# Kernel optimization log

Measured on AMD Instinct MI355X. Metric: run time of the kernel, lower is better.

## Reference

```python
import jax, jax.numpy as jnp
import numpy as np

HIDDEN = 1024
HEADS = 16
HEAD = HIDDEN // HEADS


def setup_inputs() -> dict:
    key = jax.random.key(0)
    ks = jax.random.split(key, 6)
    B, T = 2, 2048
    x = jax.random.normal(ks[0], (B, T, HIDDEN), dtype=jnp.float32)
    mask = jnp.ones((T, T), dtype=jnp.float32)
    s = 1.0 / np.sqrt(HIDDEN)
    Wqkv = jax.random.normal(ks[1], (HIDDEN, 3 * HIDDEN), dtype=jnp.float32) * s
    bqkv = jnp.zeros((3 * HIDDEN,), dtype=jnp.float32)
    Wproj = jax.random.normal(ks[2], (HIDDEN, HIDDEN), dtype=jnp.float32) * s
    bproj = jnp.zeros((HIDDEN,), dtype=jnp.float32)
    return {"x": x, "mask": mask, "Wqkv": Wqkv, "bqkv": bqkv,
            "Wproj": Wproj, "bproj": bproj}


def reference(x, mask, Wqkv, bqkv, Wproj, bproj):
    B, T, C = x.shape
    qkv = x @ Wqkv + bqkv                      # [B,T,3C]
    q, k, v = jnp.split(qkv, 3, axis=-1)
    def heads(t):                              # [B,T,C] -> [B,H,T,D]
        return t.reshape(B, T, HEADS, HEAD).transpose(0, 2, 1, 3)
    q, k, v = heads(q), heads(k), heads(v)
    scores = jnp.einsum('bhqd,bhkd->bhqk', q, k) / np.sqrt(HEAD)
    scores = jnp.where(mask == 0, -jnp.inf, scores)
    attn = jax.nn.softmax(scores, axis=-1)
    out = jnp.einsum('bhqk,bhkd->bhqd', attn, v)
    out = out.transpose(0, 2, 1, 3).reshape(B, T, C)
    return out @ Wproj + bproj
```

## Files before the change

### kernel.cpp

```cpp
#include <hip/hip_runtime.h>
#include <stdint.h>

#define HID 1024
#define NH 16
#define HD 64
#define BATCH 2
#define SEQ 2048
#define MR (BATCH*SEQ)
#define NQKV (3*HID)

typedef __attribute__((ext_vector_type(8))) _Float16 h16x8;
typedef __attribute__((ext_vector_type(4))) _Float16 h16x4;
typedef __attribute__((ext_vector_type(2))) __fp16 fp16x2;
typedef __attribute__((ext_vector_type(8))) unsigned short u16x8;
typedef __attribute__((ext_vector_type(4))) float f32x4;

#if __has_builtin(__builtin_amdgcn_exp2f)
#define EXP2(x) __builtin_amdgcn_exp2f(x)
#else
#define EXP2(x) exp2f(x)
#endif

static __device__ __forceinline__ unsigned short f2h(float f) {
  union { _Float16 h; unsigned short u; } v; v.h = (_Float16)f; return v.u;
}
static __device__ __forceinline__ unsigned pk2(float a, float b) {
  union { fp16x2 h; unsigned u; } v;
  v.h = __builtin_amdgcn_cvt_pkrtz(a, b);
  return v.u;
}

typedef const __attribute__((address_space(1))) unsigned int glb_u32;
typedef __attribute__((address_space(3))) unsigned int lds_u32;
static __device__ __forceinline__ void cp16(const void* g, void* l) {
  __builtin_amdgcn_global_load_lds((glb_u32*)g, (lds_u32*)l, 16, 0, 0);
}

#define QSCL (0.125f * 1.44269504f)

__global__ __launch_bounds__(256) void k_prep(const float4* __restrict__ x4,
                                              const float* __restrict__ mask,
                                              const float* __restrict__ Wqkv,
                                              const float* __restrict__ Wproj,
                                              ushort4* __restrict__ xh,
                                              unsigned short* __restrict__ WqT,
                                              unsigned short* __restrict__ WpT,
                                              unsigned long long* __restrict__ mb) {
  __shared__ float tile[32][33];
  int blk = blockIdx.x, tid = threadIdx.x;
  if (blk < 4096) {
    int i = blk * 256 + tid;
    float4 v = x4[i];
    ushort4 h;
    h.x = f2h(v.x); h.y = f2h(v.y); h.z = f2h(v.z); h.w = f2h(v.w);
    xh[i] = h;
  } else if (blk < 8192) {
    const float* src; unsigned short* dst; int C, bx, by;
    if (blk < 7168) { src = Wqkv;  dst = WqT; C = NQKV; int b2 = blk - 4096; bx = b2 % 96; by = b2 / 96; }
    else            { src = Wproj; dst = WpT; C = HID;  int b2 = blk - 7168; bx = b2 & 31; by = b2 >> 5; }
    int tx = tid & 31, ty = tid >> 5;
    int col0 = bx * 32, row0 = by * 32;
    #pragma unroll
    for (int i = 0; i < 32; i += 8)
      tile[ty + i][tx] = src[(size_t)(row0 + ty + i) * C + col0 + tx];
    __syncthreads();
    #pragma unroll
    for (int i = 0; i < 32; i += 8)
      dst[(size_t)(col0 + ty + i) * HID + row0 + tx] = f2h(tile[tx][ty + i]);
  } else {
    int gw0 = (blk - 8192) * 16 + (tid >> 6) * 4;
    int lane = tid & 63;
    size_t base = (size_t)gw0 * 64;
    #pragma unroll
    for (int j = 0; j < 4; j++) {
      float v = mask[base + j * 64 + lane];
      unsigned long long b = __ballot(v != 0.f);
      if (lane == 0) mb[gw0 + j] = b;
    }
  }
}

__global__ __launch_bounds__(256) void k_gemm_qkv(const unsigned short* __restrict__ A,
                                                  const unsigned short* __restrict__ Bt,
                                                  const float* __restrict__ bias,
                                                  unsigned short* __restrict__ Qp,
                                                  unsigned short* __restrict__ Kp,
                                                  unsigned short* __restrict__ Vt) {
  const int K = HID;
  int tid = threadIdx.x;
  int wave = tid >> 6, lane = tid & 63, quad = lane >> 4, l16 = lane & 15;
  int wm = wave >> 1, wn = wave & 1;
  int x7 = l16 & 7;
  int lin = blockIdx.x + 24 * blockIdx.y;
  int orig = (lin & 7) * 96 + (lin >> 3);
  int m0 = (orig / 24) * 128, n0 = (orig % 24) * 128;
  __shared__ __align__(16) unsigned short smem[17408];
  unsigned short* As = smem;
  unsigned short* Bs = smem + 8192;
  unsigned short* Lb = smem;
  f32x4 acc[4][4] = {};
  for (int k0 = 0; k0 < K; k0 += 64) {
    __syncthreads();
    #pragma unroll
    for (int i = 0; i < 4; i++) {
      int c = tid + i * 256;
      int r = c >> 3, sc = ((c ^ r) & 7) << 3;
      cp16(&A[(size_t)(m0 + r) * K + k0 + sc], &As[c << 3]);
      cp16(&Bt[(size_t)(n0 + r) * K + k0 + sc], &Bs[c << 3]);
    }
    __syncthreads();
    #pragma unroll
    for (int kc = 0; kc < 2; kc++) {
      h16x8 af[4], bf[4];
      #pragma unroll
      for (int i = 0; i < 4; i++) {
        af[i] = *(const h16x8*)&As[(wm * 64 + i * 16 + l16) * 64 + (((kc * 4 + quad) ^ x7) << 3)];
        bf[i] = *(const h16x8*)&Bs[(wn * 64 + i * 16 + l16) * 64 + (((kc * 4 + quad) ^ x7) << 3)];
      }
      #pragma unroll
      for (int i = 0; i < 4; i++)
        #pragma unroll
        for (int j = 0; j < 4; j++)
          acc[i][j] = __builtin_amdgcn_mfma_f32_16x16x32_f16(af[i], bf[j], acc[i][j], 0, 0, 0);
    }
  }
  int which = n0 >> 10;
  int hbase = (n0 & 1023) >> 6;
  __syncthreads();
  if (which == 2) {
    #pragma unroll
    for (int j = 0; j < 4; j++) {
      int nl = wn * 64 + j * 16 + l16;
      float bv = bias[n0 + nl];
      #pragma unroll
      for (int i = 0; i < 4; i++) {
        int ml = wm * 64 + i * 16 + quad * 4;
        uint2 tt;
        tt.x = pk2(acc[i][j][0] + bv, acc[i][j][1] + bv);
        tt.y = pk2(acc[i][j][2] + bv, acc[i][j][3] + bv);
        *(uint2*)&Lb[nl * 136 + ml] = tt;
      }
    }
  } else {
    float scl = (which == 0) ? QSCL : 1.0f;
    #pragma unroll
    for (int j = 0; j < 4; j++) {
      int nl = wn * 64 + j * 16 + l16;
      float bv = bias[n0 + nl];
      #pragma unroll
      for (int i = 0; i < 4; i++)
        #pragma unroll
        for (int r = 0; r < 4; r++) {
          int ml = wm * 64 + i * 16 + quad * 4 + r;
          Lb[ml * 136 + nl] = f2h((acc[i][j][r] + bv) * scl);
        }
    }
  }
  __syncthreads();
  int b = m0 >> 11, tb = m0 & 2047;
  if (which == 2) {
    #pragma unroll
    for (int p = 0; p < 8; p++) {
      int c = tid + p * 256;
      int rr = c >> 4, cc = c & 15;
      int h = hbase + (rr >> 6), d = rr & 63;
      u16x8 vv = *(const u16x8*)&Lb[rr * 136 + cc * 8];
      *(u16x8*)&Vt[(size_t)(b * NH + h) * (SEQ * HD) + (size_t)d * SEQ + tb + cc * 8] = vv;
    }
  } else {
    unsigned short* dst = (which == 0) ? Qp : Kp;
    #pragma unroll
    for (int p = 0; p < 8; p++) {
      int c = tid + p * 256;
      int rr = c >> 4, cc = c & 15;
      int h = hbase + (cc >> 3), d0 = (cc & 7) << 3;
      u16x8 vv = *(const u16x8*)&Lb[rr * 136 + cc * 8];
      *(u16x8*)&dst[(size_t)(b * NH + h) * (SEQ * HD) + (size_t)(tb + rr) * HD + d0] = vv;
    }
  }
}

__global__ __launch_bounds__(256) void k_attn(const unsigned short* __restrict__ Qp,
                                              const unsigned short* __restrict__ Kp,
                                              const unsigned short* __restrict__ Vt,
                                              const unsigned long long* __restrict__ mb,
                                              unsigned short* __restrict__ AO) {
  int tid = threadIdx.x, wave = tid >> 6, lane = tid & 63, quad = lane >> 4, l16 = lane & 15;
  int lin = blockIdx.x + 16 * blockIdx.y;
  int orig = (lin & 7) * 64 + (lin >> 3);
  int bh = orig >> 4, qbase = (orig & 15) * 128;
  const unsigned short* Qg = Qp + (size_t)bh * (SEQ * HD);
  const unsigned short* Kg = Kp + (size_t)bh * (SEQ * HD);
  const unsigned short* Vg = Vt + (size_t)bh * (SEQ * HD);
  __shared__ __align__(16) unsigned short smem[24576];
  unsigned short* Qs = smem;
  unsigned short* Os = smem;

  #pragma unroll
  for (int i = 0; i < 4; i++) {
    int c = tid + i * 256;
    int row = c >> 3, sc = ((c ^ row) & 7) << 3;
    cp16(&Qg[(size_t)(qbase + row) * HD + sc], &Qs[c << 3]);
  }
  #pragma unroll
  for (int i = 0; i < 2; i++) {
    int c = tid + i * 256;
    int row = c >> 3, sc = ((c ^ row) & 7) << 3;
    cp16(&Kg[(size_t)row * HD + sc], &smem[8192 + (c << 3)]);
    cp16(&Vg[(size_t)row * SEQ + sc], &smem[12288 + (c << 3)]);
  }
  int q0 = qbase + wave * 32 + l16;
  const unsigned long long* mrow0 = mb + (size_t)q0 * 32;
  const unsigned long long* mrow1 = mb + (size_t)(q0 + 16) * 32;
  f32x4 acc_o[2][4] = {};
  f32x4 acc_l[2] = {};
  int x7 = l16 & 7;

  h16x4 vone4;
  #pragma unroll
  for (int j = 0; j < 4; j++) vone4[j] = (_Float16)1.0f;

  __syncthreads();
  h16x8 bq[2][2];
  #pragma unroll
  for (int s = 0; s < 2; s++)
    #pragma unroll
    for (int kk = 0; kk < 2; kk++)
      bq[s][kk] = *(const h16x8*)&Qs[(wave * 32 + s * 16 + l16) * 64 + (((kk * 4 + quad) ^ x7) << 3)];

  for (int kt = 0; kt < 32; kt++) {
    unsigned short* cb = smem + 8192 + ((kt & 1) << 13);
    if (kt < 31) {
      unsigned short* nb = smem + 8192 + (((kt + 1) & 1) << 13);
      int kb2 = (kt + 1) * 64;
      #pragma unroll
      for (int i = 0; i < 2; i++) {
        int c = tid + i * 256;
        int row = c >> 3, sc = ((c ^ row) & 7) << 3;
        cp16(&Kg[(size_t)(kb2 + row) * HD + sc], &nb[c << 3]);
        cp16(&Vg[(size_t)row * SEQ + kb2 + sc], &nb[4096 + (c << 3)]);
      }
    }
    unsigned long long w0 = mrow0[kt], w1 = mrow1[kt];
    h16x8 ka[4][2];
    #pragma unroll
    for (int nt = 0; nt < 4; nt++)
      #pragma unroll
      for (int kk = 0; kk < 2; kk++)
        ka[nt][kk] = *(const h16x8*)&cb[(nt * 16 + l16) * 64 + (((kk * 4 + quad) ^ x7) << 3)];
    f32x4 s0[4] = {}, s1[4] = {};
    __builtin_amdgcn_s_setprio(1);
    #pragma unroll
    for (int nt = 0; nt < 4; nt++)
      #pragma unroll
      for (int kk = 0; kk < 2; kk++) {
        s0[nt] = __builtin_amdgcn_mfma_f32_16x16x32_f16(ka[nt][kk], bq[0][kk], s0[nt], 0, 0, 0);
        s1[nt] = __builtin_amdgcn_mfma_f32_16x16x32_f16(ka[nt][kk], bq[1][kk], s1[nt], 0, 0, 0);
      }
    __builtin_amdgcn_s_setprio(0);
    h16x4 va16[4][4];
    #pragma unroll
    for (int nt = 0; nt < 4; nt++)
      #pragma unroll
      for (int seg = 0; seg < 4; seg++)
        va16[nt][seg] = *(const h16x4*)&cb[4096 + (nt * 16 + l16) * 64 +
                                           (((seg * 2 + (quad >> 1)) ^ x7) << 3) +
                                           ((quad & 1) << 2)];
    if (!__all((w0 & w1) == ~0ULL)) {
      #pragma unroll
      for (int nt = 0; nt < 4; nt++)
        #pragma unroll
        for (int r = 0; r < 4; r++) {
          int bit = nt * 16 + quad * 4 + r;
          if (!((w0 >> bit) & 1ULL)) s0[nt][r] = -100.f;
          if (!((w1 >> bit) & 1ULL)) s1[nt][r] = -100.f;
        }
    }
    #pragma unroll
    for (int nt = 0; nt < 4; nt++)
      #pragma unroll
      for (int r = 0; r < 4; r++) {
        s0[nt][r] = EXP2(s0[nt][r]);
        s1[nt][r] = EXP2(s1[nt][r]);
      }
    auto pv = [&](const f32x4 (&s)[4], f32x4 (&ao)[4], f32x4 &al) {
      #pragma unroll
      for (int seg = 0; seg < 4; seg++) {
        union { h16x4 h; unsigned u[2]; } pb;
        pb.u[0] = pk2(s[seg][0], s[seg][1]);
        pb.u[1] = pk2(s[seg][2], s[seg][3]);
        al = __builtin_amdgcn_mfma_f32_16x16x16f16(vone4, pb.h, al, 0, 0, 0);
        #pragma unroll
        for (int nt = 0; nt < 4; nt++)
          ao[nt] = __builtin_amdgcn_mfma_f32_16x16x16f16(va16[nt][seg], pb.h, ao[nt], 0, 0, 0);
      }
    };
    __builtin_amdgcn_s_setprio(1);
    pv(s0, acc_o[0], acc_l[0]);
    pv(s1, acc_o[1], acc_l[1]);
    __builtin_amdgcn_s_setprio(0);
    asm volatile("s_waitcnt vmcnt(0)" ::: "memory");
    __builtin_amdgcn_s_barrier();
    __builtin_amdgcn_sched_barrier(0);
  }
  float rl0 = 1.0f / acc_l[0][0];
  float rl1 = 1.0f / acc_l[1][0];
  #pragma unroll
  for (int nt = 0; nt < 4; nt++) {
    uint2 t;
    t.x = (unsigned)f2h(acc_o[0][nt][0] * rl0) | ((unsigned)f2h(acc_o[0][nt][1] * rl0) << 16);
    t.y = (unsigned)f2h(acc_o[0][nt][2] * rl0) | ((unsigned)f2h(acc_o[0][nt][3] * rl0) << 16);
    *(uint2*)&Os[(wave * 32 + l16) * 72 + nt * 16 + quad * 4] = t;
    uint2 u;
    u.x = (unsigned)f2h(acc_o[1][nt][0] * rl1) | ((unsigned)f2h(acc_o[1][nt][1] * rl1) << 16);
    u.y = (unsigned)f2h(acc_o[1][nt][2] * rl1) | ((unsigned)f2h(acc_o[1][nt][3] * rl1) << 16);
    *(uint2*)&Os[(wave * 32 + 16 + l16) * 72 + nt * 16 + quad * 4] = u;
  }
  __syncthreads();
  int b = bh >> 4, h = bh & 15;
  #pragma unroll
  for (int i = 0; i < 4; i++) {
    int c = tid + i * 256;
    int row = c >> 3, co = (c & 7) << 3;
    u16x8 vv = *(const u16x8*)&Os[row * 72 + co];
    *(u16x8*)&AO[(size_t)(b * SEQ + qbase + row) * HID + h * HD + co] = vv;
  }
}

__global__ __launch_bounds__(256) void k_gemm_proj(const unsigned short* __restrict__ A,
                                                   const unsigned short* __restrict__ Bt,
                                                   const float* __restrict__ bias,
                                                   float* __restrict__ out) {
  const int K = HID;
  int tid = threadIdx.x;
  int wave = tid >> 6, lane = tid & 63, quad = lane >> 4, l16 = lane & 15;
  int wm = wave >> 1, wn = wave & 1;
  int x7 = l16 & 7;
  int lin = blockIdx.x + 16 * blockIdx.y;
  int orig = (lin & 7) * 64 + (lin >> 3);
  int m0 = (orig >> 4) * 128, n0 = (orig & 15) * 64;
  __shared__ __align__(16) unsigned short smem[17408];
  unsigned short* As = smem;
  unsigned short* Bs = smem + 8192;
  float* Lf = (float*)smem;
  f32x4 acc[4][2] = {};
  for (int k0 = 0; k0 < K; k0 += 64) {
    __syncthreads();
    #pragma unroll
    for (int i = 0; i < 4; i++) {
      int c = tid + i * 256;
      int r = c >> 3, sc = ((c ^ r) & 7) << 3;
      cp16(&A[(size_t)(m0 + r) * K + k0 + sc], &As[c << 3]);
    }
    #pragma unroll
    for (int i = 0; i < 2; i++) {
      int c = tid + i * 256;
      int r = c >> 3, sc = ((c ^ r) & 7) << 3;
      cp16(&Bt[(size_t)(n0 + r) * K + k0 + sc], &Bs[c << 3]);
    }
    __syncthreads();
    #pragma unroll
    for (int kc = 0; kc < 2; kc++) {
      h16x8 af[4], bf[2];
      #pragma unroll
      for (int i = 0; i < 4; i++)
        af[i] = *(const h16x8*)&As[(wm * 64 + i * 16 + l16) * 64 + (((kc * 4 + quad) ^ x7) << 3)];
      #pragma unroll
      for (int j = 0; j < 2; j++)
        bf[j] = *(const h16x8*)&Bs[(wn * 32 + j * 16 + l16) * 64 + (((kc * 4 + quad) ^ x7) << 3)];
      #pragma unroll
      for (int i = 0; i < 4; i++)
        #pragma unroll
        for (int j = 0; j < 2; j++)
          acc[i][j] = __builtin_amdgcn_mfma_f32_16x16x32_f16(af[i], bf[j], acc[i][j], 0, 0, 0);
    }
  }
  __syncthreads();
  #pragma unroll
  for (int j = 0; j < 2; j++) {
    int nl = wn * 32 + j * 16 + l16;
    float bv = bias[n0 + nl];
    #pragma unroll
    for (int i = 0; i < 4; i++)
      #pragma unroll
      for (int r = 0; r < 4; r++) {
        int ml = wm * 64 + i * 16 + quad * 4 + r;
        Lf[ml * 68 + nl] = acc[i][j][r] + bv;
      }
  }
  __syncthreads();
  #pragma unroll
  for (int p = 0; p < 8; p++) {
    int c = tid + p * 256;
    int rr = c >> 4, cc = c & 15;
    float4 vv = *(const float4*)&Lf[rr * 68 + cc * 4];
    *(float4*)&out[(size_t)(m0 + rr) * HID + n0 + cc * 4] = vv;
  }
}

extern "C" void kernel_launch(void* const* d_in, const int* in_sizes, int n_in,
                              void* d_out, int out_size, void* d_ws, size_t ws_size,
                              hipStream_t stream) {
  const float* x     = (const float*)d_in[0];
  const float* mask  = (const float*)d_in[1];
  const float* Wqkv  = (const float*)d_in[2];
  const float* bqkv  = (const float*)d_in[3];
  const float* Wproj = (const float*)d_in[4];
  const float* bproj = (const float*)d_in[5];
  float* out = (float*)d_out;

  uint8_t* ws = (uint8_t*)d_ws;
  size_t off = 0;
  auto alloc = [&](size_t bytes) -> void* {
    void* p = (void*)(ws + off);
    off += (bytes + 255) & ~(size_t)255;
    return p;
  };
  unsigned short* xh   = (unsigned short*)alloc((size_t)MR * HID * 2);
  unsigned short* WqT  = (unsigned short*)alloc((size_t)NQKV * HID * 2);
  unsigned short* WpT  = (unsigned short*)alloc((size_t)HID * HID * 2);
  unsigned short* Qp   = (unsigned short*)alloc((size_t)BATCH * NH * SEQ * HD * 2);
  unsigned short* Kp   = (unsigned short*)alloc((size_t)BATCH * NH * SEQ * HD * 2);
  unsigned short* Vtp  = (unsigned short*)alloc((size_t)BATCH * NH * SEQ * HD * 2);
  unsigned short* AO   = (unsigned short*)alloc((size_t)MR * HID * 2);
  unsigned long long* mb = (unsigned long long*)alloc((size_t)SEQ * (SEQ / 64) * 8);

  k_prep<<<12288, 256, 0, stream>>>((const float4*)x, mask, Wqkv, Wproj,
                                    (ushort4*)xh, WqT, WpT, mb);
  k_gemm_qkv<<<dim3(NQKV / 128, MR / 128), 256, 0, stream>>>(xh, WqT, bqkv, Qp, Kp, Vtp);
  k_attn<<<dim3(SEQ / 128, BATCH * NH), 256, 0, stream>>>(Qp, Kp, Vtp, mb, AO);
  k_gemm_proj<<<dim3(HID / 64, MR / 128), 256, 0, stream>>>(AO, WpT, bproj, out);
}
```

Before: 204.5 us.

## Double-buffer LDS tiles in QKV and projection GEMMs to overlap loads with MFMA

Both GEMM kernels now keep two shared-memory stages, so the global-to-LDS copy for the next K tile is issued before the MFMAs on the current tile run. This replaces the two barriers per K step with one waitcnt plus barrier. MFMA sections are also wrapped in s_setprio to favour the math waves. The cost is doubled LDS per block (64KB for the QKV GEMM), which may lower occupancy. The QKV launch is flattened to a 1D grid with the same tile swizzle.

```diff
diff --git a/kernel.cpp b/kernel.cpp
--- a/kernel.cpp
+++ b/kernel.cpp
@@ -86,47 +86,53 @@
                                                   unsigned short* __restrict__ Qp,
                                                   unsigned short* __restrict__ Kp,
                                                   unsigned short* __restrict__ Vt) {
-  const int K = HID;
   int tid = threadIdx.x;
   int wave = tid >> 6, lane = tid & 63, quad = lane >> 4, l16 = lane & 15;
   int wm = wave >> 1, wn = wave & 1;
   int x7 = l16 & 7;
-  int lin = blockIdx.x + 24 * blockIdx.y;
-  int orig = (lin & 7) * 96 + (lin >> 3);
+  int blk = blockIdx.x;
+  int orig = (blk & 7) * 96 + (blk >> 3);
   int m0 = (orig / 24) * 128, n0 = (orig % 24) * 128;
-  __shared__ __align__(16) unsigned short smem[17408];
-  unsigned short* As = smem;
-  unsigned short* Bs = smem + 8192;
+  __shared__ __align__(16) unsigned short smem[32768];
   unsigned short* Lb = smem;
-  f32x4 acc[4][4] = {};
-  for (int k0 = 0; k0 < K; k0 += 64) {
-    __syncthreads();
+
+  auto stage = [&](unsigned short* buf, int k0) {
     #pragma unroll
     for (int i = 0; i < 4; i++) {
       int c = tid + i * 256;
       int r = c >> 3, sc = ((c ^ r) & 7) << 3;
-      cp16(&A[(size_t)(m0 + r) * K + k0 + sc], &As[c << 3]);
-      cp16(&Bt[(size_t)(n0 + r) * K + k0 + sc], &Bs[c << 3]);
-    }
-    __syncthreads();
+      cp16(&A[(size_t)(m0 + r) * HID + k0 + sc], &buf[c << 3]);
+      cp16(&Bt[(size_t)(n0 + r) * HID + k0 + sc], &buf[8192 + (c << 3)]);
+    }
+  };
+  stage(smem, 0);
+  f32x4 acc[4][4] = {};
+  __syncthreads();
+  for (int kt = 0; kt < 16; kt++) {
+    unsigned short* cb = smem + ((kt & 1) << 14);
+    if (kt < 15) stage(smem + (((kt + 1) & 1) << 14), (kt + 1) * 64);
     #pragma unroll
     for (int kc = 0; kc < 2; kc++) {
       h16x8 af[4], bf[4];
       #pragma unroll
       for (int i = 0; i < 4; i++) {
-        af[i] = *(const h16x8*)&As[(wm * 64 + i * 16 + l16) * 64 + (((kc * 4 + quad) ^ x7) << 3)];
-        bf[i] = *(const h16x8*)&Bs[(wn * 64 + i * 16 + l16) * 64 + (((kc * 4 + quad) ^ x7) << 3)];
-      }
+        af[i] = *(const h16x8*)&cb[(wm * 64 + i * 16 + l16) * 64 + (((kc * 4 + quad) ^ x7) << 3)];
+        bf[i] = *(const h16x8*)&cb[8192 + (wn * 64 + i * 16 + l16) * 64 + (((kc * 4 + quad) ^ x7) << 3)];
+      }
+      __builtin_amdgcn_s_setprio(1);
       #pragma unroll
       for (int i = 0; i < 4; i++)
         #pragma unroll
         for (int j = 0; j < 4; j++)
           acc[i][j] = __builtin_amdgcn_mfma_f32_16x16x32_f16(af[i], bf[j], acc[i][j], 0, 0, 0);
-    }
+      __builtin_amdgcn_s_setprio(0);
+    }
+    asm volatile("s_waitcnt vmcnt(0)" ::: "memory");
+    __builtin_amdgcn_s_barrier();
+    __builtin_amdgcn_sched_barrier(0);
   }
   int which = n0 >> 10;
   int hbase = (n0 & 1023) >> 6;
-  __syncthreads();
   if (which == 2) {
     #pragma unroll
     for (int j = 0; j < 4; j++) {
@@ -331,7 +337,6 @@
                                                    const unsigned short* __restrict__ Bt,
                                                    const float* __restrict__ bias,
                                                    float* __restrict__ out) {
-  const int K = HID;
   int tid = threadIdx.x;
   int wave = tid >> 6, lane = tid & 63, quad = lane >> 4, l16 = lane & 15;
   int wm = wave >> 1, wn = wave & 1;
@@ -339,43 +344,50 @@
   int lin = blockIdx.x + 16 * blockIdx.y;
   int orig = (lin & 7) * 64 + (lin >> 3);
   int m0 = (orig >> 4) * 128, n0 = (orig & 15) * 64;
-  __shared__ __align__(16) unsigned short smem[17408];
-  unsigned short* As = smem;
-  unsigned short* Bs = smem + 8192;
+  __shared__ __align__(16) unsigned short smem[24576];
   float* Lf = (float*)smem;
-  f32x4 acc[4][2] = {};
-  for (int k0 = 0; k0 < K; k0 += 64) {
-    __syncthreads();
+
+  auto stage = [&](unsigned short* buf, int k0) {
     #pragma unroll
     for (int i = 0; i < 4; i++) {
       int c = tid + i * 256;
       int r = c >> 3, sc = ((c ^ r) & 7) << 3;
-      cp16(&A[(size_t)(m0 + r) * K + k0 + sc], &As[c << 3]);
+      cp16(&A[(size_t)(m0 + r) * HID + k0 + sc], &buf[c << 3]);
     }
     #pragma unroll
     for (int i = 0; i < 2; i++) {
       int c = tid + i * 256;
       int r = c >> 3, sc = ((c ^ r) & 7) << 3;
-      cp16(&Bt[(size_t)(n0 + r) * K + k0 + sc], &Bs[c << 3]);
-    }
-    __syncthreads();
+      cp16(&Bt[(size_t)(n0 + r) * HID + k0 + sc], &buf[8192 + (c << 3)]);
+    }
+  };
+  stage(smem, 0);
+  f32x4 acc[4][2] = {};
+  __syncthreads();
+  for (int kt = 0; kt < 16; kt++) {
+    unsigned short* cb = smem + (kt & 1) * 12288;
+    if (kt < 15) stage(smem + ((kt + 1) & 1) * 12288, (kt + 1) * 64);
     #pragma unroll
     for (int kc = 0; kc < 2; kc++) {
       h16x8 af[4], bf[2];
       #pragma unroll
       for (int i = 0; i < 4; i++)
-        af[i] = *(const h16x8*)&As[(wm * 64 + i * 16 + l16) * 64 + (((kc * 4 + quad) ^ x7) << 3)];
+        af[i] = *(const h16x8*)&cb[(wm * 64 + i * 16 + l16) * 64 + (((kc * 4 + quad) ^ x7) << 3)];
       #pragma unroll
       for (int j = 0; j < 2; j++)
-        bf[j] = *(const h16x8*)&Bs[(wn * 32 + j * 16 + l16) * 64 + (((kc * 4 + quad) ^ x7) << 3)];
+        bf[j] = *(const h16x8*)&cb[8192 + (wn * 32 + j * 16 + l16) * 64 + (((kc * 4 + quad) ^ x7) << 3)];
+      __builtin_amdgcn_s_setprio(1);
       #pragma unroll
       for (int i = 0; i < 4; i++)
         #pragma unroll
         for (int j = 0; j < 2; j++)
           acc[i][j] = __builtin_amdgcn_mfma_f32_16x16x32_f16(af[i], bf[j], acc[i][j], 0, 0, 0);
-    }
-  }
-  __syncthreads();
+      __builtin_amdgcn_s_setprio(0);
+    }
+    asm volatile("s_waitcnt vmcnt(0)" ::: "memory");
+    __builtin_amdgcn_s_barrier();
+    __builtin_amdgcn_sched_barrier(0);
+  }
   #pragma unroll
   for (int j = 0; j < 2; j++) {
     int nl = wn * 32 + j * 16 + l16;
@@ -427,7 +439,7 @@
 
   k_prep<<<12288, 256, 0, stream>>>((const float4*)x, mask, Wqkv, Wproj,
                                     (ushort4*)xh, WqT, WpT, mb);
-  k_gemm_qkv<<<dim3(NQKV / 128, MR / 128), 256, 0, stream>>>(xh, WqT, bqkv, Qp, Kp, Vtp);
+  k_gemm_qkv<<<768, 256, 0, stream>>>(xh, WqT, bqkv, Qp, Kp, Vtp);
   k_attn<<<dim3(SEQ / 128, BATCH * NH), 256, 0, stream>>>(Qp, Kp, Vtp, mb, AO);
   k_gemm_proj<<<dim3(HID / 64, MR / 128), 256, 0, stream>>>(AO, WpT, bproj, out);
 }
```

Result: no change. 205.8 us (+0.7%).
